# Kernel optimization log

Hardware: AMD Instinct MI355X
Metric: run time of the kernel (lower is better)

The kernel has to match this reference:

```python
import jax, jax.numpy as jnp
import numpy as np

N_NODES = 100000
N_EDGES = 1600000
HID = 128
MAX_Z = 1000
N_GRAPHS = 1000
N_LAYERS = 3


def setup_inputs() -> dict:
    key = jax.random.key(0)
    ks = jax.random.split(key, 10)
    z = jax.random.randint(ks[0], (N_NODES,), 0, MAX_Z)
    edge_index = jax.random.randint(ks[1], (2, N_EDGES), 0, N_NODES)
    batch = jnp.sort(jax.random.randint(ks[2], (N_NODES,), 0, N_GRAPHS))
    s = 1.0 / np.sqrt(HID)
    z_emb = jax.random.normal(ks[3], (MAX_Z, HID), jnp.float32)
    Wl = jax.random.normal(ks[4], (N_LAYERS, HID, HID), jnp.float32) * s
    bl = jnp.zeros((N_LAYERS, HID), jnp.float32)
    Wr = jax.random.normal(ks[5], (N_LAYERS, HID, HID), jnp.float32) * s
    lin1_w = jax.random.normal(ks[6], (HID, HID), jnp.float32) * s
    lin1_b = jnp.zeros((HID,), jnp.float32)
    lin2_w = jax.random.normal(ks[7], (1, HID), jnp.float32) * s
    lin2_b = jnp.zeros((1,), jnp.float32)
    return dict(z=z, edge_index=edge_index, batch=batch, num_graphs=N_GRAPHS,
                z_emb=z_emb, Wl=Wl, bl=bl, Wr=Wr,
                lin1_w=lin1_w, lin1_b=lin1_b, lin2_w=lin2_w, lin2_b=lin2_b)


def _sage_conv(x, src, dst, deg_inv, Wl_i, bl_i, Wr_i):
    # PyG SAGEConv (default): out = lin_l(mean_{j in N(i)} x_j) + lin_r(x_i)
    agg = jax.ops.segment_sum(x[src], dst, num_segments=x.shape[0]) * deg_inv[:, None]
    return agg @ Wl_i.T + bl_i + x @ Wr_i.T


def reference(z, edge_index, batch, num_graphs, z_emb, Wl, bl, Wr, lin1_w, lin1_b, lin2_w, lin2_b):
    x = z_emb[z]  # z.ndim == 1 -> z_emb.ndim == 2, no sum branch
    src, dst = edge_index[0], edge_index[1]
    n = x.shape[0]
    deg = jax.ops.segment_sum(jnp.ones((src.shape[0],), x.dtype), dst, num_segments=n)
    deg_inv = 1.0 / jnp.maximum(deg, 1.0)  # mean aggregation; empty neighborhoods -> 0
    for i in range(Wl.shape[0] - 1):
        x = jax.nn.relu(_sage_conv(x, src, dst, deg_inv, Wl[i], bl[i], Wr[i]))
        # dropout is identity in eval mode
    x = _sage_conv(x, src, dst, deg_inv, Wl[-1], bl[-1], Wr[-1])
    # batch is sorted; first occurrence of each graph id == searchsorted
    center = jnp.searchsorted(batch, jnp.arange(num_graphs))
    h = x[center] * x[center + 1]
    h = jax.nn.relu(h @ lin1_w.T + lin1_b)
    return h @ lin2_w.T + lin2_b  # [num_graphs, 1]
```

## Files before the change

### kernel.cpp

```cpp
#include <hip/hip_runtime.h>
#include <hip/hip_bf16.h>
#include <cstdint>

#define HID 128
#define GM 128
#define SCAN_CHUNK 2048

typedef __attribute__((ext_vector_type(8))) short bf16x8;
typedef __attribute__((ext_vector_type(4))) float f32x4;

__device__ __forceinline__ unsigned short f2bf(float f) {
    union { __hip_bfloat16 h; unsigned short u; } c;
    c.h = __float2bfloat16(f);
    return c.u;
}
__device__ __forceinline__ float bf2f(unsigned short u) {
    union { unsigned int i; float f; } c;
    c.i = ((unsigned int)u) << 16;
    return c.f;
}
__device__ __forceinline__ unsigned int pack2(unsigned short a, unsigned short b) {
    return (unsigned int)a | ((unsigned int)b << 16);
}
__device__ __forceinline__ bf16x8 ld_frag(const unsigned int* p) {
    union { uint4 u; bf16x8 f; } c;
    c.u = *(const uint4*)p;
    return c.f;
}

__global__ void k_count(const int* __restrict__ dst, int* __restrict__ deg,
                        int* __restrict__ slot, int n_edges) {
    int t = blockIdx.x * blockDim.x + threadIdx.x;
    int e0 = t * 4;
    if (e0 + 3 < n_edges) {
        int4 d = *(const int4*)(dst + e0);
        int4 s;
        s.x = atomicAdd(&deg[d.x], 1);
        s.y = atomicAdd(&deg[d.y], 1);
        s.z = atomicAdd(&deg[d.z], 1);
        s.w = atomicAdd(&deg[d.w], 1);
        *(int4*)(slot + e0) = s;
    } else {
        for (int e = e0; e < n_edges; ++e) slot[e] = atomicAdd(&deg[dst[e]], 1);
    }
}

__global__ void k_scan1(const int* __restrict__ v_in, int* __restrict__ partials, int n) {
    __shared__ int sm[256];
    int t = threadIdx.x;
    int base = blockIdx.x * SCAN_CHUNK + t * 8;
    int s = 0;
#pragma unroll
    for (int j = 0; j < 8; ++j) { int i = base + j; if (i < n) s += v_in[i]; }
    sm[t] = s;
    __syncthreads();
    for (int off = 128; off > 0; off >>= 1) {
        if (t < off) sm[t] += sm[t + off];
        __syncthreads();
    }
    if (t == 0) partials[blockIdx.x] = sm[0];
}

__global__ void k_scan2(int* partials, int nchunks, int* total) {
    int lane = threadIdx.x;
    int v = (lane < nchunks) ? partials[lane] : 0;
#pragma unroll
    for (int off = 1; off < 64; off <<= 1) {
        int u = __shfl_up(v, off);
        if (lane >= off) v += u;
    }
    if (total && lane == nchunks - 1) *total = v;
    int ex = __shfl_up(v, 1);
    if (lane == 0) ex = 0;
    if (lane < nchunks) partials[lane] = ex;
}

__global__ void k_scan3(const int* __restrict__ deg, const int* __restrict__ partials,
                        int* __restrict__ rowptr, float* __restrict__ deg_inv, int n) {
    __shared__ int wtot[4];
    int t = threadIdx.x;
    int lane = t & 63, wv = t >> 6;
    int base = blockIdx.x * SCAN_CHUNK + t * 8;
    int v[8];
    int ts = 0;
#pragma unroll
    for (int j = 0; j < 8; ++j) { int i = base + j; v[j] = (i < n) ? deg[i] : 0; ts += v[j]; }
    int incl = ts;
#pragma unroll
    for (int off = 1; off < 64; off <<= 1) {
        int u = __shfl_up(incl, off);
        if (lane >= off) incl += u;
    }
    if (lane == 63) wtot[wv] = incl;
    __syncthreads();
    int woff = 0;
    for (int w = 0; w < wv; ++w) woff += wtot[w];
    int run = partials[blockIdx.x] + woff + (incl - ts);
#pragma unroll
    for (int j = 0; j < 8; ++j) {
        int i = base + j;
        run += v[j];
        if (i < n) {
            rowptr[i + 1] = run;
            deg_inv[i] = 1.0f / fmaxf((float)v[j], 1.0f);
        }
    }
    if (blockIdx.x == 0 && t == 0) rowptr[0] = 0;
}

__global__ void k_compact(const int* __restrict__ flag, const int* __restrict__ partials,
                          int* __restrict__ remap, int* __restrict__ nodes2, int n) {
    __shared__ int wtot[4];
    int t = threadIdx.x;
    int lane = t & 63, wv = t >> 6;
    int base = blockIdx.x * SCAN_CHUNK + t * 8;
    int v[8];
    int ts = 0;
#pragma unroll
    for (int j = 0; j < 8; ++j) { int i = base + j; v[j] = (i < n) ? flag[i] : 0; ts += v[j]; }
    int incl = ts;
#pragma unroll
    for (int off = 1; off < 64; off <<= 1) {
        int u = __shfl_up(incl, off);
        if (lane >= off) incl += u;
    }
    if (lane == 63) wtot[wv] = incl;
    __syncthreads();
    int woff = 0;
    for (int w = 0; w < wv; ++w) woff += wtot[w];
    int run = partials[blockIdx.x] + woff + (incl - ts);
#pragma unroll
    for (int j = 0; j < 8; ++j) {
        int i = base + j;
        if (i < n) {
            remap[i] = run;
            if (v[j]) nodes2[run] = i;
        }
        run += v[j];
    }
}

__global__ void k_fill(const int* __restrict__ src, const int* __restrict__ dst,
                       const int* __restrict__ slot, const int* __restrict__ rowptr,
                       const int* __restrict__ z, int2* __restrict__ csr2, int n_edges) {
    int t = blockIdx.x * blockDim.x + threadIdx.x;
    int e0 = t * 4;
    if (e0 + 3 < n_edges) {
        int4 d  = *(const int4*)(dst + e0);
        int4 s  = *(const int4*)(src + e0);
        int4 sl = *(const int4*)(slot + e0);
        int p0 = rowptr[d.x] + sl.x;
        int p1 = rowptr[d.y] + sl.y;
        int p2 = rowptr[d.z] + sl.z;
        int p3 = rowptr[d.w] + sl.w;
        csr2[p0] = make_int2(s.x, z[s.x]);
        csr2[p1] = make_int2(s.y, z[s.y]);
        csr2[p2] = make_int2(s.z, z[s.z]);
        csr2[p3] = make_int2(s.w, z[s.w]);
    } else {
        for (int e = e0; e < n_edges; ++e) {
            int se = src[e];
            csr2[rowptr[dst[e]] + slot[e]] = make_int2(se, z[se]);
        }
    }
}

__global__ void k_zlr(const float* __restrict__ z_emb, const float* __restrict__ Wl,
                      const float* __restrict__ Wr, const float* __restrict__ bl,
                      float* __restrict__ zl, float* __restrict__ zr, int max_z) {
    __shared__ float row[HID];
    int r = blockIdx.x;
    if (r >= max_z) return;
    int t = threadIdx.x;
    if (t < HID) row[t] = z_emb[(size_t)r * HID + t];
    __syncthreads();
    int d = t & 127;
    const float* w = (t < 128 ? Wl : Wr) + (size_t)d * HID;
    float acc = 0.f;
#pragma unroll
    for (int k4 = 0; k4 < HID / 4; ++k4) {
        float4 wv = *(const float4*)(w + k4 * 4);
        float4 hv = *(const float4*)&row[k4 * 4];
        acc += wv.x * hv.x + wv.y * hv.y + wv.z * hv.z + wv.w * hv.w;
    }
    if (t < 128) zl[(size_t)r * HID + d] = acc;
    else         zr[(size_t)r * HID + d] = acc + bl[d];
}

__global__ void k_flag(const int* __restrict__ sel, const int* __restrict__ rowptr,
                       const int2* __restrict__ csr2, int* __restrict__ flag, int n_sel) {
    int r = (blockIdx.x * blockDim.x + threadIdx.x) >> 6;
    int lane = threadIdx.x & 63;
    if (r >= n_sel) return;
    int node = sel[r];
    if (lane == 0) flag[node] = 1;
    int s = rowptr[node], e = rowptr[node + 1];
    for (int i = s + lane; i < e; i += 64) flag[csr2[i].x] = 1;
}

__global__ void k_selremap(const int* __restrict__ sel, const int* __restrict__ remap,
                           int* __restrict__ selr, int n_sel) {
    int i = blockIdx.x * blockDim.x + threadIdx.x;
    if (i < n_sel) selr[i] = remap[sel[i]];
}

template<int MODE>
__global__ __launch_bounds__(256) void k_agg(const float* __restrict__ xv_,
                      float* __restrict__ aggout,
                      const int* __restrict__ rowptr, const int2* __restrict__ csr2,
                      const float* __restrict__ deg_inv, const int* __restrict__ idxmap,
                      const int* __restrict__ remap,
                      const int* __restrict__ z, const float* __restrict__ zr,
                      int n_host, const int* __restrict__ n_dev) {
    int nw_total = gridDim.x * 4;
    int w0 = blockIdx.x * 4 + (threadIdx.x >> 6);
    int lane = threadIdx.x & 63;
    int n = n_dev ? *n_dev : n_host;
    int half = lane >> 5;
    int col = lane & 31;
    const float4* xv = (const float4*)xv_;
    for (int r = w0; r < n; r += nw_total) {
        int node = (MODE == 1) ? r : idxmap[r];
        int s = rowptr[node], e = rowptr[node + 1];
        float4 a0 = {0.f,0.f,0.f,0.f}, a1 = {0.f,0.f,0.f,0.f};
        float4 a2 = {0.f,0.f,0.f,0.f}, a3 = {0.f,0.f,0.f,0.f};
        int i = s + half;
        for (; i + 6 < e; i += 8) {
            int2 c0 = csr2[i];
            int2 c1 = csr2[i + 2];
            int2 c2 = csr2[i + 4];
            int2 c3 = csr2[i + 6];
            int s0 = (MODE == 1) ? c0.y : c0.x;
            int s1 = (MODE == 1) ? c1.y : c1.x;
            int s2 = (MODE == 1) ? c2.y : c2.x;
            int s3 = (MODE == 1) ? c3.y : c3.x;
            if (MODE == 3) { s0 = remap[s0]; s1 = remap[s1]; s2 = remap[s2]; s3 = remap[s3]; }
            float4 v0 = xv[(size_t)s0 * 32 + col];
            float4 v1 = xv[(size_t)s1 * 32 + col];
            float4 v2 = xv[(size_t)s2 * 32 + col];
            float4 v3 = xv[(size_t)s3 * 32 + col];
            a0.x += v0.x; a0.y += v0.y; a0.z += v0.z; a0.w += v0.w;
            a1.x += v1.x; a1.y += v1.y; a1.z += v1.z; a1.w += v1.w;
            a2.x += v2.x; a2.y += v2.y; a2.z += v2.z; a2.w += v2.w;
            a3.x += v3.x; a3.y += v3.y; a3.z += v3.z; a3.w += v3.w;
        }
        for (; i < e; i += 2) {
            int2 c0 = csr2[i];
            int s0 = (MODE == 1) ? c0.y : c0.x;
            if (MODE == 3) s0 = remap[s0];
            float4 v0 = xv[(size_t)s0 * 32 + col];
            a0.x += v0.x; a0.y += v0.y; a0.z += v0.z; a0.w += v0.w;
        }
        a0.x += a1.x + a2.x + a3.x;
        a0.y += a1.y + a2.y + a3.y;
        a0.z += a1.z + a2.z + a3.z;
        a0.w += a1.w + a2.w + a3.w;
        a0.x += __shfl_xor(a0.x, 32);
        a0.y += __shfl_xor(a0.y, 32);
        a0.z += __shfl_xor(a0.z, 32);
        a0.w += __shfl_xor(a0.w, 32);
        if (half == 0) {
            float di = deg_inv[node];
            float4 o = make_float4(a0.x * di, a0.y * di, a0.z * di, a0.w * di);
            if (MODE == 1) {
                int zn = z[node];
                float4 rv = ((const float4*)zr)[(size_t)zn * 32 + col];
                o.x = fmaxf(o.x + rv.x, 0.f);
                o.y = fmaxf(o.y + rv.y, 0.f);
                o.z = fmaxf(o.z + rv.z, 0.f);
                o.w = fmaxf(o.w + rv.w, 0.f);
            }
            ((float4*)aggout)[(size_t)r * 32 + col] = o;
        }
    }
}

__global__ void k_wsplit(const float* __restrict__ Wl, const float* __restrict__ Wr,
                         unsigned short* __restrict__ wh, unsigned short* __restrict__ wlo) {
    int idx = blockIdx.x * blockDim.x + threadIdx.x;
    if (idx >= 3 * HID * 2 * HID) return;
    int l = idx / (HID * 2 * HID);
    int r = idx - l * (HID * 2 * HID);
    int d = r >> 8;
    int k = r & 255;
    float v = (k < HID) ? Wl[((size_t)l * HID + d) * HID + k]
                        : Wr[((size_t)l * HID + d) * HID + (k - HID)];
    unsigned short h = f2bf(v);
    unsigned short lo = f2bf(v - bf2f(h));
    wh[idx] = h;
    wlo[idx] = lo;
}

__global__ __launch_bounds__(256) void k_gemm(const float* __restrict__ aggsrc,
                                              const float* __restrict__ xsrc,
                                              float* __restrict__ out,
                                              const unsigned short* __restrict__ wh,
                                              const unsigned short* __restrict__ wlo,
                                              const float* __restrict__ bias,
                                              const int* __restrict__ xidx,
                                              int n_host, const int* __restrict__ n_dev,
                                              int do_relu) {
    __shared__ unsigned int sAh[GM * 16], sAl[GM * 16];
    __shared__ unsigned int sBh[HID * 16], sBl[HID * 16];
    int n_rows = n_dev ? *n_dev : n_host;
    int t = threadIdx.x;
    int node0 = blockIdx.x * GM;
    if (node0 >= n_rows) return;
    int wv = t >> 6, lane = t & 63;
    int lrow = lane & 15, lk = lane >> 4;

    f32x4 acc[2][8];
#pragma unroll
    for (int m = 0; m < 2; ++m)
#pragma unroll
        for (int n = 0; n < 8; ++n) acc[m][n] = (f32x4){0.f, 0.f, 0.f, 0.f};

    int srow = t >> 2;
    int sq = t & 3;

    int gg[2] = {node0 + srow, node0 + srow + 64};
    bool vv[2] = {gg[0] < n_rows, gg[1] < n_rows};
    int xr[2];
#pragma unroll
    for (int rr = 0; rr < 2; ++rr)
        xr[rr] = xidx ? (vv[rr] ? xidx[gg[rr]] : 0) : gg[rr];

    for (int c = 0; c < 8; ++c) {
        int kbase = (c & 3) * 32;
        int kb = c * 32;
#pragma unroll
        for (int rr = 0; rr < 2; ++rr) {
            int row = srow + rr * 64;
            const float* srcrow = (c < 4) ? aggsrc + (size_t)gg[rr] * HID
                                          : xsrc + (size_t)xr[rr] * HID;
            float f[8];
            if (vv[rr]) {
                const float4* rp = (const float4*)(srcrow + kbase + sq * 8);
                float4 v0 = rp[0], v1 = rp[1];
                f[0]=v0.x; f[1]=v0.y; f[2]=v0.z; f[3]=v0.w;
                f[4]=v1.x; f[5]=v1.y; f[6]=v1.z; f[7]=v1.w;
            } else {
#pragma unroll
                for (int j = 0; j < 8; ++j) f[j] = 0.f;
            }
            unsigned int h[4], l[4];
#pragma unroll
            for (int j = 0; j < 4; ++j) {
                unsigned short h0 = f2bf(f[2*j]), h1 = f2bf(f[2*j+1]);
                unsigned short l0 = f2bf(f[2*j] - bf2f(h0));
                unsigned short l1 = f2bf(f[2*j+1] - bf2f(h1));
                h[j] = pack2(h0, h1);
                l[j] = pack2(l0, l1);
            }
            unsigned int base = row * 16 + sq * 4;
            *(uint4*)&sAh[base] = make_uint4(h[0], h[1], h[2], h[3]);
            *(uint4*)&sAl[base] = make_uint4(l[0], l[1], l[2], l[3]);
        }
#pragma unroll
        for (int rr = 0; rr < 2; ++rr) {
            int d = srow + rr * 64;
            size_t go = (size_t)d * 256 + kb + sq * 8;
            uint4 vh = *(const uint4*)(wh + go);
            uint4 vl = *(const uint4*)(wlo + go);
            unsigned int base = d * 16 + sq * 4;
            *(uint4*)&sBh[base] = vh;
            *(uint4*)&sBl[base] = vl;
        }
        __syncthreads();
        bf16x8 ah0, al0, ah1, al1;
        {
            unsigned int a0 = (unsigned)(wv * 32 + lrow) * 16 + lk * 4;
            unsigned int a1 = (unsigned)(wv * 32 + 16 + lrow) * 16 + lk * 4;
            ah0 = ld_frag(&sAh[a0]); al0 = ld_frag(&sAl[a0]);
            ah1 = ld_frag(&sAh[a1]); al1 = ld_frag(&sAl[a1]);
        }
#pragma unroll
        for (int n = 0; n < 8; ++n) {
            unsigned int b = (unsigned)(n * 16 + lrow) * 16 + lk * 4;
            bf16x8 bh = ld_frag(&sBh[b]);
            bf16x8 bl = ld_frag(&sBl[b]);
            acc[0][n] = __builtin_amdgcn_mfma_f32_16x16x32_bf16(ah0, bh, acc[0][n], 0, 0, 0);
            acc[0][n] = __builtin_amdgcn_mfma_f32_16x16x32_bf16(al0, bh, acc[0][n], 0, 0, 0);
            acc[0][n] = __builtin_amdgcn_mfma_f32_16x16x32_bf16(ah0, bl, acc[0][n], 0, 0, 0);
            acc[1][n] = __builtin_amdgcn_mfma_f32_16x16x32_bf16(ah1, bh, acc[1][n], 0, 0, 0);
            acc[1][n] = __builtin_amdgcn_mfma_f32_16x16x32_bf16(al1, bh, acc[1][n], 0, 0, 0);
            acc[1][n] = __builtin_amdgcn_mfma_f32_16x16x32_bf16(ah1, bl, acc[1][n], 0, 0, 0);
        }
        __syncthreads();
    }
#pragma unroll
    for (int m = 0; m < 2; ++m) {
        int rbase = node0 + wv * 32 + m * 16 + lk * 4;
#pragma unroll
        for (int n = 0; n < 8; ++n) {
            int colb = n * 16 + lrow;
            float bb = bias[colb];
#pragma unroll
            for (int r = 0; r < 4; ++r) {
                int row = rbase + r;
                if (row < n_rows) {
                    float v = acc[m][n][r] + bb;
                    if (do_relu) v = fmaxf(v, 0.f);
                    out[(size_t)row * HID + colb] = v;
                }
            }
        }
    }
}

__global__ void k_center(const int* __restrict__ batch, int* __restrict__ sel,
                         int n_nodes, int n_graphs) {
    int g = blockIdx.x * blockDim.x + threadIdx.x;
    if (g >= n_graphs) return;
    int lo = 0, hi = n_nodes;
    while (lo < hi) {
        int mid = (lo + hi) >> 1;
        if (batch[mid] < g) lo = mid + 1;
        else hi = mid;
    }
    sel[2 * g]     = min(lo, n_nodes - 1);
    sel[2 * g + 1] = min(lo + 1, n_nodes - 1);
}

__global__ void k_readout(const float* __restrict__ y,
                          const float* __restrict__ w1, const float* __restrict__ b1,
                          const float* __restrict__ w2, const float* __restrict__ b2,
                          float* __restrict__ out, int n_graphs) {
    __shared__ float h[HID];
    int g = blockIdx.x;
    if (g >= n_graphs) return;
    int lane = threadIdx.x;
    float2 a = ((const float2*)(y + (size_t)(2 * g) * HID))[lane];
    float2 b = ((const float2*)(y + (size_t)(2 * g + 1) * HID))[lane];
    h[2 * lane] = a.x * b.x;
    h[2 * lane + 1] = a.y * b.y;
    __syncthreads();
    int d0 = 2 * lane;
    float acc0 = b1[d0], acc1 = b1[d0 + 1];
    const float4* w1a = (const float4*)(w1 + (size_t)d0 * HID);
    const float4* w1b = (const float4*)(w1 + (size_t)(d0 + 1) * HID);
#pragma unroll 8
    for (int k4 = 0; k4 < HID / 4; ++k4) {
        float4 hv = *(const float4*)&h[k4 * 4];
        float4 wa = w1a[k4];
        float4 wb = w1b[k4];
        acc0 += hv.x * wa.x + hv.y * wa.y + hv.z * wa.z + hv.w * wa.w;
        acc1 += hv.x * wb.x + hv.y * wb.y + hv.z * wb.z + hv.w * wb.w;
    }
    float p = fmaxf(acc0, 0.f) * w2[d0] + fmaxf(acc1, 0.f) * w2[d0 + 1];
#pragma unroll
    for (int off = 32; off > 0; off >>= 1) p += __shfl_down(p, off);
    if (lane == 0) out[g] = p + b2[0];
}

extern "C" void kernel_launch(void* const* d_in, const int* in_sizes, int n_in,
                              void* d_out, int out_size, void* d_ws, size_t ws_size,
                              hipStream_t stream) {
    const int* z = (const int*)d_in[0];
    const int* edge_index = (const int*)d_in[1];
    const int* batch = (const int*)d_in[2];
    const float* z_emb = (const float*)d_in[4];
    const float* Wl = (const float*)d_in[5];
    const float* bl = (const float*)d_in[6];
    const float* Wr = (const float*)d_in[7];
    const float* lin1_w = (const float*)d_in[8];
    const float* lin1_b = (const float*)d_in[9];
    const float* lin2_w = (const float*)d_in[10];
    const float* lin2_b = (const float*)d_in[11];
    float* out = (float*)d_out;

    int n_nodes = in_sizes[0];
    int n_edges = in_sizes[1] / 2;
    int max_z = in_sizes[4] / HID;
    int n_graphs = out_size;
    int n_sel = 2 * n_graphs;

    const int* e_src = edge_index;
    const int* e_dst = edge_index + n_edges;

    char* p = (char*)d_ws;
    auto alloc = [&](size_t bytes) {
        char* r = p;
        p += (bytes + 511) & ~(size_t)511;
        return r;
    };
    float* x      = (float*)alloc((size_t)n_nodes * HID * 4);
    float* agg2   = (float*)alloc((size_t)n_nodes * HID * 4);
    float* x2c    = (float*)alloc((size_t)n_nodes * HID * 4);
    float* aggsel = (float*)alloc((size_t)n_sel * HID * 4);
    float* y      = (float*)alloc((size_t)n_sel * HID * 4);
    int*   deg    = (int*)alloc((size_t)n_nodes * 4);
    float* deginv = (float*)alloc((size_t)n_nodes * 4);
    int*   rowptr = (int*)alloc((size_t)(n_nodes + 1) * 4);
    int*   slot   = (int*)alloc((size_t)n_edges * 4);
    int2*  csr2   = (int2*)alloc((size_t)n_edges * 8);
    int*   parts  = (int*)alloc(64 * 4);
    int*   sel    = (int*)alloc((size_t)n_sel * 4);
    int*   selr   = (int*)alloc((size_t)n_sel * 4);
    int*   flag   = (int*)alloc((size_t)n_nodes * 4);
    int*   remap  = (int*)alloc((size_t)n_nodes * 4);
    int*   nodes2 = (int*)alloc((size_t)n_nodes * 4);
    int*   n2     = (int*)alloc(4);
    float* zl     = (float*)alloc((size_t)max_z * HID * 4);
    float* zr     = (float*)alloc((size_t)max_z * HID * 4);
    unsigned short* wh  = (unsigned short*)alloc((size_t)3 * HID * 2 * HID * 2);
    unsigned short* wlo = (unsigned short*)alloc((size_t)3 * HID * 2 * HID * 2);

    hipMemsetAsync(deg, 0, (size_t)n_nodes * 4, stream);
    hipMemsetAsync(flag, 0, (size_t)n_nodes * 4, stream);

    k_wsplit<<<(3 * HID * 2 * HID + 255) / 256, 256, 0, stream>>>(Wl, Wr, wh, wlo);
    k_zlr<<<max_z, 256, 0, stream>>>(z_emb, Wl, Wr, bl, zl, zr, max_z);

    int n4 = (n_edges + 3) / 4;
    k_count<<<(n4 + 255) / 256, 256, 0, stream>>>(e_dst, deg, slot, n_edges);

    int nchunks = (n_nodes + SCAN_CHUNK - 1) / SCAN_CHUNK;
    k_scan1<<<nchunks, 256, 0, stream>>>(deg, parts, n_nodes);
    k_scan2<<<1, 64, 0, stream>>>(parts, nchunks, nullptr);
    k_scan3<<<nchunks, 256, 0, stream>>>(deg, parts, rowptr, deginv, n_nodes);

    k_fill<<<(n4 + 255) / 256, 256, 0, stream>>>(e_src, e_dst, slot, rowptr, z, csr2, n_edges);
    k_center<<<(n_graphs + 255) / 256, 256, 0, stream>>>(batch, sel, n_nodes, n_graphs);

    k_flag<<<(n_sel * 64 + 255) / 256, 256, 0, stream>>>(sel, rowptr, csr2, flag, n_sel);
    k_scan1<<<nchunks, 256, 0, stream>>>(flag, parts, n_nodes);
    k_scan2<<<1, 64, 0, stream>>>(parts, nchunks, n2);
    k_compact<<<nchunks, 256, 0, stream>>>(flag, parts, remap, nodes2, n_nodes);
    k_selremap<<<(n_sel + 255) / 256, 256, 0, stream>>>(sel, remap, selr, n_sel);

    int agg_blocks = (n_nodes + 3) / 4;
    k_agg<1><<<agg_blocks, 256, 0, stream>>>(zl, x, rowptr, csr2, deginv, nullptr,
                                             nullptr, z, zr, n_nodes, nullptr);
    k_agg<2><<<2048, 256, 0, stream>>>(x, agg2, rowptr, csr2, deginv, nodes2,
                                       nullptr, nullptr, nullptr, 0, n2);
    k_gemm<<<(n_nodes + GM - 1) / GM, 256, 0, stream>>>(agg2, x, x2c,
                                            wh + (size_t)HID * 2 * HID,
                                            wlo + (size_t)HID * 2 * HID,
                                            bl + HID, nodes2, 0, n2, 1);
    k_agg<3><<<(n_sel + 3) / 4, 256, 0, stream>>>(x2c, aggsel, rowptr, csr2, deginv, sel,
                                                  remap, nullptr, nullptr, n_sel, nullptr);
    k_gemm<<<(n_sel + GM - 1) / GM, 256, 0, stream>>>(aggsel, x2c, y,
                                                      wh + (size_t)2 * HID * 2 * HID,
                                                      wlo + (size_t)2 * HID * 2 * HID,
                                                      bl + (size_t)2 * HID,
                                                      selr, n_sel, nullptr, 0);
    k_readout<<<n_graphs, 64, 0, stream>>>(y, lin1_w, lin1_b, lin2_w, lin2_b, out, n_graphs);
}
```

Baseline: 313.9 us.

## Build CSR via two-pass radix binning instead of global atomic counting

Replaces the global-atomic degree count, scan and scatter fill with a radix-style build. A per-block shared-memory histogram on the low 9 bits of dst is followed by a column scan and a routing pass into 512 bins, then a per-bin grouping by the high bits that writes csr2, start and deg. This removes 1.6M contended global atomics and the random scatter writes, at the cost of more kernel launches and an extra edge buffer round trip. CSR ordering within a row becomes nondeterministic, and rows are now located by start/deg with deg_inv computed inline.

```diff
diff --git a/kernel.cpp b/kernel.cpp
--- a/kernel.cpp
+++ b/kernel.cpp
@@ -5,6 +5,9 @@
 #define HID 128
 #define GM 128
 #define SCAN_CHUNK 2048
+#define NBIN 512
+#define CHUNK 2048
+#define MAXHI 1024
 
 typedef __attribute__((ext_vector_type(8))) short bf16x8;
 typedef __attribute__((ext_vector_type(4))) float f32x4;
@@ -28,20 +31,129 @@
     return c.f;
 }
 
-__global__ void k_count(const int* __restrict__ dst, int* __restrict__ deg,
-                        int* __restrict__ slot, int n_edges) {
-    int t = blockIdx.x * blockDim.x + threadIdx.x;
-    int e0 = t * 4;
-    if (e0 + 3 < n_edges) {
-        int4 d = *(const int4*)(dst + e0);
-        int4 s;
-        s.x = atomicAdd(&deg[d.x], 1);
-        s.y = atomicAdd(&deg[d.y], 1);
-        s.z = atomicAdd(&deg[d.z], 1);
-        s.w = atomicAdd(&deg[d.w], 1);
-        *(int4*)(slot + e0) = s;
-    } else {
-        for (int e = e0; e < n_edges; ++e) slot[e] = atomicAdd(&deg[dst[e]], 1);
+__device__ __forceinline__ int block_scan_excl(int v, int t, int* wtot, int* tot) {
+    int lane = t & 63, wv = t >> 6;
+    int incl = v;
+#pragma unroll
+    for (int off = 1; off < 64; off <<= 1) {
+        int u = __shfl_up(incl, off);
+        if (lane >= off) incl += u;
+    }
+    if (lane == 63) wtot[wv] = incl;
+    __syncthreads();
+    int woff = 0;
+    for (int w = 0; w < wv; ++w) woff += wtot[w];
+    if (tot) *tot = wtot[0] + wtot[1] + wtot[2] + wtot[3];
+    __syncthreads();
+    return woff + incl - v;
+}
+
+__global__ __launch_bounds__(256) void k_hist(const int* __restrict__ dst,
+                                              int* __restrict__ hist, int n_edges) {
+    __shared__ int h[NBIN];
+    int t = threadIdx.x;
+    h[t] = 0; h[t + 256] = 0;
+    __syncthreads();
+    int base = blockIdx.x * CHUNK;
+#pragma unroll
+    for (int j = 0; j < CHUNK / 256; ++j) {
+        int e = base + j * 256 + t;
+        if (e < n_edges) atomicAdd(&h[dst[e] & (NBIN - 1)], 1);
+    }
+    __syncthreads();
+    hist[(size_t)blockIdx.x * NBIN + t] = h[t];
+    hist[(size_t)blockIdx.x * NBIN + t + 256] = h[t + 256];
+}
+
+__global__ __launch_bounds__(256) void k_colscan(int* __restrict__ hist,
+                                                 int* __restrict__ bintotal, int B) {
+    __shared__ int wtot[4];
+    int k = blockIdx.x, t = threadIdx.x;
+    int run = 0;
+    for (int base = 0; base < B; base += 256) {
+        int b = base + t;
+        int v = (b < B) ? hist[(size_t)b * NBIN + k] : 0;
+        int tot;
+        int excl = block_scan_excl(v, t, wtot, &tot);
+        if (b < B) hist[(size_t)b * NBIN + k] = run + excl;
+        run += tot;
+    }
+    if (t == 0) bintotal[k] = run;
+}
+
+__global__ __launch_bounds__(256) void k_binbase(const int* __restrict__ bintotal,
+                                                 int* __restrict__ binbase) {
+    __shared__ int wtot[4];
+    int t = threadIdx.x;
+    int a0 = bintotal[2 * t], a1 = bintotal[2 * t + 1];
+    int excl = block_scan_excl(a0 + a1, t, wtot, nullptr);
+    binbase[2 * t] = excl;
+    binbase[2 * t + 1] = excl + a0;
+    if (t == 255) binbase[NBIN] = excl + a0 + a1;
+}
+
+__global__ __launch_bounds__(256) void k_route(const int* __restrict__ src,
+                                               const int* __restrict__ dst,
+                                               const int* __restrict__ histex,
+                                               const int* __restrict__ binbase,
+                                               int2* __restrict__ ebuf, int n_edges) {
+    __shared__ int h2[NBIN];
+    __shared__ int basel[NBIN];
+    int t = threadIdx.x;
+    h2[t] = 0; h2[t + 256] = 0;
+    basel[t]       = binbase[t]       + histex[(size_t)blockIdx.x * NBIN + t];
+    basel[t + 256] = binbase[t + 256] + histex[(size_t)blockIdx.x * NBIN + t + 256];
+    __syncthreads();
+    int base = blockIdx.x * CHUNK;
+#pragma unroll
+    for (int j = 0; j < CHUNK / 256; ++j) {
+        int e = base + j * 256 + t;
+        if (e < n_edges) {
+            int d = dst[e], s = src[e];
+            int bin = d & (NBIN - 1);
+            int r = atomicAdd(&h2[bin], 1);
+            ebuf[basel[bin] + r] = make_int2(s, d);
+        }
+    }
+}
+
+__global__ __launch_bounds__(256) void k_group(const int2* __restrict__ ebuf,
+                                               const int* __restrict__ binbase,
+                                               const int* __restrict__ z,
+                                               int2* __restrict__ csr2,
+                                               int* __restrict__ start, int* __restrict__ deg,
+                                               int n_nodes) {
+    __shared__ int hh[MAXHI];
+    __shared__ int cur[MAXHI];
+    __shared__ int wtot[4];
+    int k = blockIdx.x, t = threadIdx.x;
+    int rs = binbase[k], re = binbase[k + 1];
+#pragma unroll
+    for (int j = 0; j < MAXHI / 256; ++j) hh[t + j * 256] = 0;
+    __syncthreads();
+    for (int i = rs + t; i < re; i += 256)
+        atomicAdd(&hh[ebuf[i].y >> 9], 1);
+    __syncthreads();
+    int idx = t * 4;
+    int a0 = hh[idx], a1 = hh[idx + 1], a2 = hh[idx + 2], a3 = hh[idx + 3];
+    int excl = block_scan_excl(a0 + a1 + a2 + a3, t, wtot, nullptr);
+    int e0 = excl, e1 = e0 + a0, e2 = e1 + a1, e3 = e2 + a2;
+    cur[idx] = e0; cur[idx + 1] = e1; cur[idx + 2] = e2; cur[idx + 3] = e3;
+    int ee[4] = {e0, e1, e2, e3};
+    int aa[4] = {a0, a1, a2, a3};
+#pragma unroll
+    for (int j = 0; j < 4; ++j) {
+        int node = ((idx + j) << 9) | k;
+        if (node < n_nodes) {
+            start[node] = rs + ee[j];
+            deg[node] = aa[j];
+        }
+    }
+    __syncthreads();
+    for (int i = rs + t; i < re; i += 256) {
+        int2 sd = ebuf[i];
+        int r = atomicAdd(&cur[sd.y >> 9], 1);
+        csr2[rs + r] = make_int2(sd.x, z[sd.x]);
     }
 }
 
@@ -73,39 +185,6 @@
     int ex = __shfl_up(v, 1);
     if (lane == 0) ex = 0;
     if (lane < nchunks) partials[lane] = ex;
-}
-
-__global__ void k_scan3(const int* __restrict__ deg, const int* __restrict__ partials,
-                        int* __restrict__ rowptr, float* __restrict__ deg_inv, int n) {
-    __shared__ int wtot[4];
-    int t = threadIdx.x;
-    int lane = t & 63, wv = t >> 6;
-    int base = blockIdx.x * SCAN_CHUNK + t * 8;
-    int v[8];
-    int ts = 0;
-#pragma unroll
-    for (int j = 0; j < 8; ++j) { int i = base + j; v[j] = (i < n) ? deg[i] : 0; ts += v[j]; }
-    int incl = ts;
-#pragma unroll
-    for (int off = 1; off < 64; off <<= 1) {
-        int u = __shfl_up(incl, off);
-        if (lane >= off) incl += u;
-    }
-    if (lane == 63) wtot[wv] = incl;
-    __syncthreads();
-    int woff = 0;
-    for (int w = 0; w < wv; ++w) woff += wtot[w];
-    int run = partials[blockIdx.x] + woff + (incl - ts);
-#pragma unroll
-    for (int j = 0; j < 8; ++j) {
-        int i = base + j;
-        run += v[j];
-        if (i < n) {
-            rowptr[i + 1] = run;
-            deg_inv[i] = 1.0f / fmaxf((float)v[j], 1.0f);
-        }
-    }
-    if (blockIdx.x == 0 && t == 0) rowptr[0] = 0;
 }
 
 __global__ void k_compact(const int* __restrict__ flag, const int* __restrict__ partials,
@@ -140,31 +219,6 @@
     }
 }
 
-__global__ void k_fill(const int* __restrict__ src, const int* __restrict__ dst,
-                       const int* __restrict__ slot, const int* __restrict__ rowptr,
-                       const int* __restrict__ z, int2* __restrict__ csr2, int n_edges) {
-    int t = blockIdx.x * blockDim.x + threadIdx.x;
-    int e0 = t * 4;
-    if (e0 + 3 < n_edges) {
-        int4 d  = *(const int4*)(dst + e0);
-        int4 s  = *(const int4*)(src + e0);
-        int4 sl = *(const int4*)(slot + e0);
-        int p0 = rowptr[d.x] + sl.x;
-        int p1 = rowptr[d.y] + sl.y;
-        int p2 = rowptr[d.z] + sl.z;
-        int p3 = rowptr[d.w] + sl.w;
-        csr2[p0] = make_int2(s.x, z[s.x]);
-        csr2[p1] = make_int2(s.y, z[s.y]);
-        csr2[p2] = make_int2(s.z, z[s.z]);
-        csr2[p3] = make_int2(s.w, z[s.w]);
-    } else {
-        for (int e = e0; e < n_edges; ++e) {
-            int se = src[e];
-            csr2[rowptr[dst[e]] + slot[e]] = make_int2(se, z[se]);
-        }
-    }
-}
-
 __global__ void k_zlr(const float* __restrict__ z_emb, const float* __restrict__ Wl,
                       const float* __restrict__ Wr, const float* __restrict__ bl,
                       float* __restrict__ zl, float* __restrict__ zr, int max_z) {
@@ -187,14 +241,15 @@
     else         zr[(size_t)r * HID + d] = acc + bl[d];
 }
 
-__global__ void k_flag(const int* __restrict__ sel, const int* __restrict__ rowptr,
+__global__ void k_flag(const int* __restrict__ sel, const int* __restrict__ start,
+                       const int* __restrict__ deg,
                        const int2* __restrict__ csr2, int* __restrict__ flag, int n_sel) {
     int r = (blockIdx.x * blockDim.x + threadIdx.x) >> 6;
     int lane = threadIdx.x & 63;
     if (r >= n_sel) return;
     int node = sel[r];
     if (lane == 0) flag[node] = 1;
-    int s = rowptr[node], e = rowptr[node + 1];
+    int s = start[node], e = s + deg[node];
     for (int i = s + lane; i < e; i += 64) flag[csr2[i].x] = 1;
 }
 
@@ -207,9 +262,9 @@
 template<int MODE>
 __global__ __launch_bounds__(256) void k_agg(const float* __restrict__ xv_,
                       float* __restrict__ aggout,
-                      const int* __restrict__ rowptr, const int2* __restrict__ csr2,
-                      const float* __restrict__ deg_inv, const int* __restrict__ idxmap,
-                      const int* __restrict__ remap,
+                      const int* __restrict__ start, const int* __restrict__ deg,
+                      const int2* __restrict__ csr2,
+                      const int* __restrict__ idxmap, const int* __restrict__ remap,
                       const int* __restrict__ z, const float* __restrict__ zr,
                       int n_host, const int* __restrict__ n_dev) {
     int nw_total = gridDim.x * 4;
@@ -221,7 +276,9 @@
     const float4* xv = (const float4*)xv_;
     for (int r = w0; r < n; r += nw_total) {
         int node = (MODE == 1) ? r : idxmap[r];
-        int s = rowptr[node], e = rowptr[node + 1];
+        int s = start[node];
+        int dg = deg[node];
+        int e = s + dg;
         float4 a0 = {0.f,0.f,0.f,0.f}, a1 = {0.f,0.f,0.f,0.f};
         float4 a2 = {0.f,0.f,0.f,0.f}, a3 = {0.f,0.f,0.f,0.f};
         int i = s + half;
@@ -260,7 +317,7 @@
         a0.z += __shfl_xor(a0.z, 32);
         a0.w += __shfl_xor(a0.w, 32);
         if (half == 0) {
-            float di = deg_inv[node];
+            float di = 1.0f / fmaxf((float)dg, 1.0f);
             float4 o = make_float4(a0.x * di, a0.y * di, a0.z * di, a0.w * di);
             if (MODE == 1) {
                 int zn = z[node];
@@ -490,10 +547,13 @@
     float* aggsel = (float*)alloc((size_t)n_sel * HID * 4);
     float* y      = (float*)alloc((size_t)n_sel * HID * 4);
     int*   deg    = (int*)alloc((size_t)n_nodes * 4);
-    float* deginv = (float*)alloc((size_t)n_nodes * 4);
-    int*   rowptr = (int*)alloc((size_t)(n_nodes + 1) * 4);
-    int*   slot   = (int*)alloc((size_t)n_edges * 4);
+    int*   start  = (int*)alloc((size_t)n_nodes * 4);
+    int2*  ebuf   = (int2*)alloc((size_t)n_edges * 8);
     int2*  csr2   = (int2*)alloc((size_t)n_edges * 8);
+    int B = (n_edges + CHUNK - 1) / CHUNK;
+    int*   hist     = (int*)alloc((size_t)B * NBIN * 4);
+    int*   bintotal = (int*)alloc((size_t)NBIN * 4);
+    int*   binbase  = (int*)alloc((size_t)(NBIN + 1) * 4);
     int*   parts  = (int*)alloc(64 * 4);
     int*   sel    = (int*)alloc((size_t)n_sel * 4);
     int*   selr   = (int*)alloc((size_t)n_sel * 4);
@@ -506,39 +566,36 @@
     unsigned short* wh  = (unsigned short*)alloc((size_t)3 * HID * 2 * HID * 2);
     unsigned short* wlo = (unsigned short*)alloc((size_t)3 * HID * 2 * HID * 2);
 
-    hipMemsetAsync(deg, 0, (size_t)n_nodes * 4, stream);
     hipMemsetAsync(flag, 0, (size_t)n_nodes * 4, stream);
 
     k_wsplit<<<(3 * HID * 2 * HID + 255) / 256, 256, 0, stream>>>(Wl, Wr, wh, wlo);
     k_zlr<<<max_z, 256, 0, stream>>>(z_emb, Wl, Wr, bl, zl, zr, max_z);
 
-    int n4 = (n_edges + 3) / 4;
-    k_count<<<(n4 + 255) / 256, 256, 0, stream>>>(e_dst, deg, slot, n_edges);
-
+    k_hist<<<B, 256, 0, stream>>>(e_dst, hist, n_edges);
+    k_colscan<<<NBIN, 256, 0, stream>>>(hist, bintotal, B);
+    k_binbase<<<1, 256, 0, stream>>>(bintotal, binbase);
+    k_route<<<B, 256, 0, stream>>>(e_src, e_dst, hist, binbase, ebuf, n_edges);
+    k_group<<<NBIN, 256, 0, stream>>>(ebuf, binbase, z, csr2, start, deg, n_nodes);
+
+    k_center<<<(n_graphs + 255) / 256, 256, 0, stream>>>(batch, sel, n_nodes, n_graphs);
+
+    k_flag<<<(n_sel * 64 + 255) / 256, 256, 0, stream>>>(sel, start, deg, csr2, flag, n_sel);
     int nchunks = (n_nodes + SCAN_CHUNK - 1) / SCAN_CHUNK;
-    k_scan1<<<nchunks, 256, 0, stream>>>(deg, parts, n_nodes);
-    k_scan2<<<1, 64, 0, stream>>>(parts, nchunks, nullptr);
-    k_scan3<<<nchunks, 256, 0, stream>>>(deg, parts, rowptr, deginv, n_nodes);
-
-    k_fill<<<(n4 + 255) / 256, 256, 0, stream>>>(e_src, e_dst, slot, rowptr, z, csr2, n_edges);
-    k_center<<<(n_graphs + 255) / 256, 256, 0, stream>>>(batch, sel, n_nodes, n_graphs);
-
-    k_flag<<<(n_sel * 64 + 255) / 256, 256, 0, stream>>>(sel, rowptr, csr2, flag, n_sel);
     k_scan1<<<nchunks, 256, 0, stream>>>(flag, parts, n_nodes);
     k_scan2<<<1, 64, 0, stream>>>(parts, nchunks, n2);
     k_compact<<<nchunks, 256, 0, stream>>>(flag, parts, remap, nodes2, n_nodes);
     k_selremap<<<(n_sel + 255) / 256, 256, 0, stream>>>(sel, remap, selr, n_sel);
 
     int agg_blocks = (n_nodes + 3) / 4;
-    k_agg<1><<<agg_blocks, 256, 0, stream>>>(zl, x, rowptr, csr2, deginv, nullptr,
+    k_agg<1><<<agg_blocks, 256, 0, stream>>>(zl, x, start, deg, csr2, nullptr,
                                              nullptr, z, zr, n_nodes, nullptr);
-    k_agg<2><<<2048, 256, 0, stream>>>(x, agg2, rowptr, csr2, deginv, nodes2,
+    k_agg<2><<<2048, 256, 0, stream>>>(x, agg2, start, deg, csr2, nodes2,
                                        nullptr, nullptr, nullptr, 0, n2);
     k_gemm<<<(n_nodes + GM - 1) / GM, 256, 0, stream>>>(agg2, x, x2c,
                                             wh + (size_t)HID * 2 * HID,
                                             wlo + (size_t)HID * 2 * HID,
                                             bl + HID, nodes2, 0, n2, 1);
-    k_agg<3><<<(n_sel + 3) / 4, 256, 0, stream>>>(x2c, aggsel, rowptr, csr2, deginv, sel,
+    k_agg<3><<<(n_sel + 3) / 4, 256, 0, stream>>>(x2c, aggsel, start, deg, csr2, sel,
                                                   remap, nullptr, nullptr, n_sel, nullptr);
     k_gemm<<<(n_sel + GM - 1) / GM, 256, 0, stream>>>(aggsel, x2c, y,
                                                       wh + (size_t)2 * HID * 2 * HID,
```

New measurement: 261.6 us. 1.2x faster.
